# Performance work log

Hardware: AMD Instinct MI355X
Metric: run time of the kernel (lower is better)

The kernel has to match this reference:

```python
import jax, jax.numpy as jnp
import numpy as np

N_NODES = 50000
N_EDGES = 400000
D_IN = 512
D_OUT = 512
MASK_RATE = 0.3


def setup_inputs() -> dict:
    key = jax.random.key(0)
    k1, k2, k3, k4, k5 = jax.random.split(key, 5)
    feat = jax.random.normal(k1, (N_NODES, D_IN), dtype=jnp.float32)
    # xavier_uniform for weight [in_feat, out_feat]
    limit = float(np.sqrt(6.0 / (D_IN + D_OUT)))
    weight = jax.random.uniform(k2, (D_IN, D_OUT), dtype=jnp.float32, minval=-limit, maxval=limit)
    edge_src = jax.random.randint(k3, (N_EDGES,), 0, N_NODES, dtype=jnp.int64 if jax.config.jax_enable_x64 else jnp.int32)
    edge_dst = jax.random.randint(k4, (N_EDGES,), 0, N_NODES, dtype=jnp.int64 if jax.config.jax_enable_x64 else jnp.int32)
    edge_val = jax.random.uniform(k5, (N_EDGES,), dtype=jnp.float32)
    # deterministic stand-in for torch.randperm(...)[:num_mask]
    perm = jax.random.permutation(jax.random.fold_in(key, 7), N_NODES)
    mask_idx = perm[: int(MASK_RATE * N_NODES)]
    return {
        "feat": feat,
        "weight": weight,
        "edge_val": edge_val,
        "edge_src": edge_src,
        "edge_dst": edge_dst,
        "mask_idx": mask_idx,
    }


def reference(feat, weight, edge_val, edge_src, edge_dst, mask_idx):
    # zero out masked node rows (encoding_mask_noise)
    out_x = feat.at[mask_idx].set(0.0)
    # dense transform: [N, D_in] @ [D_in, D_out]
    x = out_x @ weight
    # spmm(adj, x): for edge (src -> dst, val): out[dst] += val * x[src]
    msgs = edge_val[:, None] * x[edge_src]  # [E, D_out]
    out = jax.ops.segment_sum(msgs, edge_dst, num_segments=feat.shape[0])
    return out, mask_idx
```

## Files before the change

### kernel.cpp

```cpp
#include <hip/hip_runtime.h>

#define DD 512
#define SCAN_B 256
#define BM 128
#define BN 128
#define BK 32
#define NSTEP 16
typedef unsigned short u16;
typedef unsigned int u32;
typedef unsigned char u8;

typedef __attribute__((ext_vector_type(8))) __bf16 bf16v8;
typedef __attribute__((ext_vector_type(2))) __bf16 bf16v2;
typedef __attribute__((ext_vector_type(4))) float f32x4;

__device__ __forceinline__ u32 pk2(float a, float b) {
  bf16v2 v;
  v[0] = (__bf16)a;
  v[1] = (__bf16)b;
  return __builtin_bit_cast(u32, v);
}
__device__ __forceinline__ u16 f2bf(float f) {
  return __builtin_bit_cast(u16, (__bf16)f);
}
__device__ __forceinline__ float bf2f(u32 h) {
  return __builtin_bit_cast(float, h << 16);
}

typedef const __attribute__((address_space(1))) void* gptr_t;
typedef __attribute__((address_space(3))) void* lptr_t;
__device__ __forceinline__ void gload_lds16(const void* g, void* l) {
  __builtin_amdgcn_global_load_lds((gptr_t)g, (lptr_t)l, 16, 0, 0);
}

#define BAR_N(N)                                                        \
  do {                                                                  \
    __builtin_amdgcn_sched_barrier(0);                                  \
    asm volatile("s_waitcnt vmcnt(" #N ") lgkmcnt(0)\n\ts_barrier" ::: "memory"); \
  } while (0)

__global__ __launch_bounds__(256) void wconv_t(const float* __restrict__ W,
                                               u16* __restrict__ Wt) {
  __shared__ float sm[64][65];
  const int bx = blockIdx.x;
  const int by = blockIdx.y;
  const int t = threadIdx.x;
  const int r = t >> 6;
  const int c = t & 63;
#pragma unroll
  for (int i = 0; i < 64; i += 4)
    sm[i + r][c] = W[(size_t)(bx * 64 + i + r) * DD + by * 64 + c];
  __syncthreads();
#pragma unroll
  for (int i = 0; i < 64; i += 4) {
    const int n = by * 64 + i + r;
    const int k = bx * 64 + c;
    Wt[(size_t)n * DD + k] = f2bf(sm[c][i + r]);
  }
}

__global__ __launch_bounds__(512) void gemm_pipe(const float* __restrict__ A,
                                                 const u16* __restrict__ Bt,
                                                 u16* __restrict__ X,
                                                 const u8* __restrict__ flg, int M) {
  __shared__ __align__(16) u16 ldsA[2][BM * BK];
  __shared__ __align__(16) u16 ldsB[3][BN * BK];
  const int tid = threadIdx.x;
  const int lane = tid & 63;
  const int w = tid >> 6;
  const int wm = w >> 2;
  const int wn = w & 3;

  const int nwg = gridDim.x;
  const int b = blockIdx.x;
  const int xcd = b & 7, j = b >> 3;
  const int q = nwg >> 3, r_ = nwg & 7;
  const int unit = (xcd < r_ ? xcd * (q + 1) : r_ * (q + 1) + (xcd - r_) * q) + j;
  const int row0 = (unit >> 2) * BM;
  const int colB = (unit & 3) * BN;

  const int lr = lane & 15;
  const int kg = lane >> 4;

  f32x4 acc[4][2] = {};

  const int arow = tid >> 2;
  const int agk = (tid & 3) ^ ((arow >> 1) & 3);
  int ar = row0 + arow;
  if (ar >= M) ar = M - 1;
  const float* gA = A + (size_t)ar * DD + agk * 8;
  const int laoff = tid * 8;
  const u32 akeep = flg[ar] ? 0u : 0xFFFFFFFFu;

  const int bcol = tid >> 2;
  const int bgk = (tid & 3) ^ ((bcol >> 1) & 3);
  const u16* gB = Bt + (size_t)(colB + bcol) * DD + bgk * 8;
  const int lboff = tid * 8;

  f32x4 rP[2][2];

  gload_lds16(gB, &ldsB[0][lboff]);
  gload_lds16(gB + BK, &ldsB[1][lboff]);
  rP[0][0] = *(const f32x4*)(gA);
  rP[0][1] = *(const f32x4*)(gA + 4);
  rP[1][0] = *(const f32x4*)(gA + BK);
  rP[1][1] = *(const f32x4*)(gA + BK + 4);
  {
    uint4 pk;
    pk.x = pk2(rP[0][0].x, rP[0][0].y) & akeep;
    pk.y = pk2(rP[0][0].z, rP[0][0].w) & akeep;
    pk.z = pk2(rP[0][1].x, rP[0][1].y) & akeep;
    pk.w = pk2(rP[0][1].z, rP[0][1].w) & akeep;
    *(uint4*)&ldsA[0][laoff] = pk;
  }
  BAR_N(2);

#pragma unroll
  for (int t = 0; t < NSTEP; ++t) {
    if (t + 2 < NSTEP)
      gload_lds16(gB + (t + 2) * BK, &ldsB[(t + 2) % 3][lboff]);
    if (t + 2 < NSTEP) {
      rP[t & 1][0] = *(const f32x4*)(gA + (t + 2) * BK);
      rP[t & 1][1] = *(const f32x4*)(gA + (t + 2) * BK + 4);
    }
    __builtin_amdgcn_sched_barrier(0);

    bf16v8 af[4], bfr[2];
#pragma unroll
    for (int m = 0; m < 4; ++m) {
      const int row = wm * 64 + m * 16 + lr;
      const int kc = kg ^ ((row >> 1) & 3);
      af[m] = *(const bf16v8*)&ldsA[t & 1][row * BK + kc * 8];
    }
#pragma unroll
    for (int n = 0; n < 2; ++n) {
      const int col = wn * 32 + n * 16 + lr;
      const int kc = kg ^ ((col >> 1) & 3);
      bfr[n] = *(const bf16v8*)&ldsB[t % 3][col * BK + kc * 8];
    }
#pragma unroll
    for (int m = 0; m < 4; ++m)
#pragma unroll
      for (int n = 0; n < 2; ++n)
        acc[m][n] = __builtin_amdgcn_mfma_f32_16x16x32_bf16(af[m], bfr[n], acc[m][n], 0, 0, 0);

    if (t + 1 < NSTEP) {
      uint4 pk;
      pk.x = pk2(rP[(t + 1) & 1][0].x, rP[(t + 1) & 1][0].y) & akeep;
      pk.y = pk2(rP[(t + 1) & 1][0].z, rP[(t + 1) & 1][0].w) & akeep;
      pk.z = pk2(rP[(t + 1) & 1][1].x, rP[(t + 1) & 1][1].y) & akeep;
      pk.w = pk2(rP[(t + 1) & 1][1].z, rP[(t + 1) & 1][1].w) & akeep;
      *(uint4*)&ldsA[(t + 1) & 1][laoff] = pk;
    }

    if (t < NSTEP - 3)      BAR_N(3);
    else if (t < NSTEP - 1) BAR_N(0);
  }

  const int crow = (lane >> 4) * 4;
  const int ccol = lane & 15;
#pragma unroll
  for (int m = 0; m < 4; ++m) {
    const int rowb = row0 + wm * 64 + m * 16 + crow;
#pragma unroll
    for (int n = 0; n < 2; ++n) {
      const int col = colB + wn * 32 + n * 16 + ccol;
#pragma unroll
      for (int r = 0; r < 4; ++r)
        X[(size_t)(rowb + r) * DD + col] = f2bf(acc[m][n][r]);
    }
  }
}

__global__ __launch_bounds__(256) void flag_build(const int* __restrict__ mask,
                                                  u8* __restrict__ flg,
                                                  float* __restrict__ out_tail, int nm) {
  const int i = blockIdx.x * blockDim.x + threadIdx.x;
  if (i < nm) {
    const int r = mask[i];
    flg[r] = 1;
    out_tail[i] = (float)r;
  }
}

__global__ __launch_bounds__(256) void hist(const int* __restrict__ dst,
                                            int* __restrict__ counts, int n) {
  const int i = blockIdx.x * blockDim.x + threadIdx.x;
  if (i < n) atomicAdd(&counts[dst[i]], 1);
}

__global__ __launch_bounds__(SCAN_B) void scanA(const int* __restrict__ counts,
                                                int* __restrict__ lscan,
                                                int* __restrict__ blockSums, int n) {
  __shared__ int sm[SCAN_B];
  const int t = threadIdx.x;
  const int i = blockIdx.x * SCAN_B + t;
  const int v = (i < n) ? counts[i] : 0;
  sm[t] = v;
  __syncthreads();
  for (int off = 1; off < SCAN_B; off <<= 1) {
    int add = (t >= off) ? sm[t - off] : 0;
    __syncthreads();
    sm[t] += add;
    __syncthreads();
  }
  if (i < n) lscan[i] = sm[t] - v;
  if (t == SCAN_B - 1) blockSums[blockIdx.x] = sm[t];
}

__global__ __launch_bounds__(SCAN_B) void scanC(int* __restrict__ lscan,
                                                const int* __restrict__ blockSums,
                                                int* __restrict__ cursor, int n, int nb) {
  __shared__ int sm[SCAN_B];
  const int t = threadIdx.x;
  const int v = (t < nb) ? blockSums[t] : 0;
  sm[t] = v;
  __syncthreads();
  for (int off = 1; off < SCAN_B; off <<= 1) {
    int add = (t >= off) ? sm[t - off] : 0;
    __syncthreads();
    sm[t] += add;
    __syncthreads();
  }
  const int base = sm[blockIdx.x] - ((blockIdx.x < nb) ? blockSums[blockIdx.x] : 0);
  const int i = blockIdx.x * SCAN_B + t;
  if (i < n) {
    const int o = lscan[i] + base;
    lscan[i] = o;
    cursor[i] = o;
  }
}

__global__ __launch_bounds__(256) void scatter_sort(const int* __restrict__ src,
                                                    const int* __restrict__ dst,
                                                    const float* __restrict__ ev,
                                                    int* __restrict__ cursor,
                                                    int* __restrict__ ssrc,
                                                    float* __restrict__ sval, int n) {
  const int i = blockIdx.x * blockDim.x + threadIdx.x;
  if (i < n) {
    const int pos = atomicAdd(&cursor[dst[i]], 1);
    ssrc[pos] = src[i];
    sval[pos] = ev[i];
  }
}

__global__ __launch_bounds__(256) void aggregate(const u16* __restrict__ x,
                                                 const int* __restrict__ ssrc,
                                                 const float* __restrict__ sval,
                                                 const int* __restrict__ offsets,
                                                 const int* __restrict__ counts,
                                                 float* __restrict__ out, int n_nodes) {
  const int node = blockIdx.x * 4 + (threadIdx.x >> 6);
  if (node >= n_nodes) return;
  const int lane = threadIdx.x & 63;
  const int b = offsets[node];
  const int e = b + counts[node];
  float acc[8] = {};
  int j = b;
#define AGG1(U, V)                                      \
  do {                                                  \
    acc[0] = fmaf(V, bf2f(U.x & 0xffffu), acc[0]);      \
    acc[1] = fmaf(V, bf2f(U.x >> 16),     acc[1]);      \
    acc[2] = fmaf(V, bf2f(U.y & 0xffffu), acc[2]);      \
    acc[3] = fmaf(V, bf2f(U.y >> 16),     acc[3]);      \
    acc[4] = fmaf(V, bf2f(U.z & 0xffffu), acc[4]);      \
    acc[5] = fmaf(V, bf2f(U.z >> 16),     acc[5]);      \
    acc[6] = fmaf(V, bf2f(U.w & 0xffffu), acc[6]);      \
    acc[7] = fmaf(V, bf2f(U.w >> 16),     acc[7]);      \
  } while (0)
  for (; j + 4 <= e; j += 4) {
    const int s0 = ssrc[j], s1 = ssrc[j + 1], s2 = ssrc[j + 2], s3 = ssrc[j + 3];
    const float v0 = sval[j], v1 = sval[j + 1], v2 = sval[j + 2], v3 = sval[j + 3];
    const uint4 u0 = *(const uint4*)(x + (size_t)s0 * DD + lane * 8);
    const uint4 u1 = *(const uint4*)(x + (size_t)s1 * DD + lane * 8);
    const uint4 u2 = *(const uint4*)(x + (size_t)s2 * DD + lane * 8);
    const uint4 u3 = *(const uint4*)(x + (size_t)s3 * DD + lane * 8);
    AGG1(u0, v0); AGG1(u1, v1); AGG1(u2, v2); AGG1(u3, v3);
  }
  for (; j < e; ++j) {
    const int s = ssrc[j];
    const float v = sval[j];
    const uint4 u = *(const uint4*)(x + (size_t)s * DD + lane * 8);
    AGG1(u, v);
  }
#undef AGG1
  f32x4* o = (f32x4*)(out + (size_t)node * DD + lane * 8);
  f32x4 o0 = {acc[0], acc[1], acc[2], acc[3]};
  f32x4 o1 = {acc[4], acc[5], acc[6], acc[7]};
  __builtin_nontemporal_store(o0, o);
  __builtin_nontemporal_store(o1, o + 1);
}

extern "C" void kernel_launch(void* const* d_in, const int* in_sizes, int n_in,
                              void* d_out, int out_size, void* d_ws, size_t ws_size,
                              hipStream_t stream) {
  const float* feat     = (const float*)d_in[0];
  const float* weight   = (const float*)d_in[1];
  const float* edge_val = (const float*)d_in[2];
  const int*   edge_src = (const int*)d_in[3];
  const int*   edge_dst = (const int*)d_in[4];
  const int*   mask_idx = (const int*)d_in[5];

  const int n_nodes = in_sizes[0] / DD;
  const int n_edges = in_sizes[2];
  const int n_mask  = in_sizes[5];

  const int n_tiles_m = (n_nodes + BM - 1) / BM;
  const int m_pad = n_tiles_m * BM;

  float* out = (float*)d_out;

  char* base = (char*)d_ws;
  size_t off = 0;
  auto alloc = [&](size_t bytes) {
    void* p = base + off;
    off = (off + bytes + 255) & ~(size_t)255;
    return p;
  };
  u16*   x      = (u16*)alloc((size_t)m_pad * DD * sizeof(u16));
  u16*   wt     = (u16*)alloc((size_t)DD * DD * sizeof(u16));
  int*   counts = (int*)alloc((size_t)n_nodes * sizeof(int));
  u8*    flg    = (u8*)alloc((size_t)m_pad);
  const size_t zspan = (size_t)((char*)(flg + m_pad) - (char*)counts);
  int*   offs   = (int*)alloc((size_t)n_nodes * sizeof(int));
  int*   cursor = (int*)alloc((size_t)n_nodes * sizeof(int));
  int*   bsums  = (int*)alloc(SCAN_B * sizeof(int));
  int*   ssrc   = (int*)alloc((size_t)n_edges * sizeof(int));
  float* sval   = (float*)alloc((size_t)n_edges * sizeof(float));

  const int nb = (n_nodes + SCAN_B - 1) / SCAN_B;

  (void)hipMemsetAsync(counts, 0, zspan, stream);
  hist<<<(n_edges + 255) / 256, 256, 0, stream>>>(edge_dst, counts, n_edges);
  scanA<<<nb, SCAN_B, 0, stream>>>(counts, offs, bsums, n_nodes);
  scanC<<<nb, SCAN_B, 0, stream>>>(offs, bsums, cursor, n_nodes, nb);
  scatter_sort<<<(n_edges + 255) / 256, 256, 0, stream>>>(edge_src, edge_dst, edge_val,
                                                          cursor, ssrc, sval, n_edges);
  flag_build<<<(n_mask + 255) / 256, 256, 0, stream>>>(mask_idx, flg,
                                                       out + (size_t)n_nodes * DD, n_mask);

  dim3 wg(DD / 64, DD / 64);
  wconv_t<<<wg, 256, 0, stream>>>(weight, wt);
  const int nwg = (DD / BN) * n_tiles_m;
  gemm_pipe<<<nwg, 512, 0, stream>>>(feat, wt, x, flg, n_nodes);

  aggregate<<<(n_nodes + 3) / 4, 256, 0, stream>>>(x, ssrc, sval, offs, counts, out, n_nodes);
}
```

Baseline: 179.9 us.

## Load GEMM B fragments directly from global, pack edges, fuse hist and flag kernels

The GEMM no longer stages the transposed weight tile in LDS. Each wave reads its B fragments straight from global memory into registers, and the A prefetch ring grows to three slots with a shallower barrier wait. Launch bounds now ask for higher occupancy. Edge src and val are packed into one int2 array so the aggregate does a single load per edge and unrolls by 8 for more gathers in flight. The histogram and mask-flag kernels are fused into one launch. The risk is uncoalesced, redundant global B reads (each wave rereads B with no LDS sharing) and more register pressure.

```diff
diff --git a/kernel.cpp b/kernel.cpp
--- a/kernel.cpp
+++ b/kernel.cpp
@@ -27,12 +27,6 @@
   return __builtin_bit_cast(float, h << 16);
 }
 
-typedef const __attribute__((address_space(1))) void* gptr_t;
-typedef __attribute__((address_space(3))) void* lptr_t;
-__device__ __forceinline__ void gload_lds16(const void* g, void* l) {
-  __builtin_amdgcn_global_load_lds((gptr_t)g, (lptr_t)l, 16, 0, 0);
-}
-
 #define BAR_N(N)                                                        \
   do {                                                                  \
     __builtin_amdgcn_sched_barrier(0);                                  \
@@ -59,12 +53,11 @@
   }
 }
 
-__global__ __launch_bounds__(512) void gemm_pipe(const float* __restrict__ A,
-                                                 const u16* __restrict__ Bt,
-                                                 u16* __restrict__ X,
-                                                 const u8* __restrict__ flg, int M) {
+__global__ __launch_bounds__(512, 4) void gemm_pipe(const float* __restrict__ A,
+                                                    const u16* __restrict__ Bt,
+                                                    u16* __restrict__ X,
+                                                    const u8* __restrict__ flg, int M) {
   __shared__ __align__(16) u16 ldsA[2][BM * BK];
-  __shared__ __align__(16) u16 ldsB[3][BN * BK];
   const int tid = threadIdx.x;
   const int lane = tid & 63;
   const int w = tid >> 6;
@@ -73,9 +66,9 @@
 
   const int nwg = gridDim.x;
   const int b = blockIdx.x;
-  const int xcd = b & 7, j = b >> 3;
+  const int xcd = b & 7, jj = b >> 3;
   const int q = nwg >> 3, r_ = nwg & 7;
-  const int unit = (xcd < r_ ? xcd * (q + 1) : r_ * (q + 1) + (xcd - r_) * q) + j;
+  const int unit = (xcd < r_ ? xcd * (q + 1) : r_ * (q + 1) + (xcd - r_) * q) + jj;
   const int row0 = (unit >> 2) * BM;
   const int colB = (unit & 3) * BN;
 
@@ -92,15 +85,11 @@
   const int laoff = tid * 8;
   const u32 akeep = flg[ar] ? 0u : 0xFFFFFFFFu;
 
-  const int bcol = tid >> 2;
-  const int bgk = (tid & 3) ^ ((bcol >> 1) & 3);
-  const u16* gB = Bt + (size_t)(colB + bcol) * DD + bgk * 8;
-  const int lboff = tid * 8;
-
-  f32x4 rP[2][2];
-
-  gload_lds16(gB, &ldsB[0][lboff]);
-  gload_lds16(gB + BK, &ldsB[1][lboff]);
+  const u16* gB0 = Bt + (size_t)(colB + wn * 32 + lr) * DD + kg * 8;
+  const u16* gB1 = Bt + (size_t)(colB + wn * 32 + 16 + lr) * DD + kg * 8;
+
+  f32x4 rP[3][2];
+
   rP[0][0] = *(const f32x4*)(gA);
   rP[0][1] = *(const f32x4*)(gA + 4);
   rP[1][0] = *(const f32x4*)(gA + BK);
@@ -117,15 +106,16 @@
 
 #pragma unroll
   for (int t = 0; t < NSTEP; ++t) {
-    if (t + 2 < NSTEP)
-      gload_lds16(gB + (t + 2) * BK, &ldsB[(t + 2) % 3][lboff]);
+    bf16v8 bfr[2];
+    bfr[0] = *(const bf16v8*)(gB0 + t * BK);
+    bfr[1] = *(const bf16v8*)(gB1 + t * BK);
+
     if (t + 2 < NSTEP) {
-      rP[t & 1][0] = *(const f32x4*)(gA + (t + 2) * BK);
-      rP[t & 1][1] = *(const f32x4*)(gA + (t + 2) * BK + 4);
+      rP[(t + 2) % 3][0] = *(const f32x4*)(gA + (t + 2) * BK);
+      rP[(t + 2) % 3][1] = *(const f32x4*)(gA + (t + 2) * BK + 4);
     }
-    __builtin_amdgcn_sched_barrier(0);
-
-    bf16v8 af[4], bfr[2];
+
+    bf16v8 af[4];
 #pragma unroll
     for (int m = 0; m < 4; ++m) {
       const int row = wm * 64 + m * 16 + lr;
@@ -133,27 +123,23 @@
       af[m] = *(const bf16v8*)&ldsA[t & 1][row * BK + kc * 8];
     }
 #pragma unroll
-    for (int n = 0; n < 2; ++n) {
-      const int col = wn * 32 + n * 16 + lr;
-      const int kc = kg ^ ((col >> 1) & 3);
-      bfr[n] = *(const bf16v8*)&ldsB[t % 3][col * BK + kc * 8];
-    }
-#pragma unroll
     for (int m = 0; m < 4; ++m)
 #pragma unroll
       for (int n = 0; n < 2; ++n)
         acc[m][n] = __builtin_amdgcn_mfma_f32_16x16x32_bf16(af[m], bfr[n], acc[m][n], 0, 0, 0);
 
     if (t + 1 < NSTEP) {
+      const f32x4 p0 = rP[(t + 1) % 3][0];
+      const f32x4 p1 = rP[(t + 1) % 3][1];
       uint4 pk;
-      pk.x = pk2(rP[(t + 1) & 1][0].x, rP[(t + 1) & 1][0].y) & akeep;
-      pk.y = pk2(rP[(t + 1) & 1][0].z, rP[(t + 1) & 1][0].w) & akeep;
-      pk.z = pk2(rP[(t + 1) & 1][1].x, rP[(t + 1) & 1][1].y) & akeep;
-      pk.w = pk2(rP[(t + 1) & 1][1].z, rP[(t + 1) & 1][1].w) & akeep;
+      pk.x = pk2(p0.x, p0.y) & akeep;
+      pk.y = pk2(p0.z, p0.w) & akeep;
+      pk.z = pk2(p1.x, p1.y) & akeep;
+      pk.w = pk2(p1.z, p1.w) & akeep;
       *(uint4*)&ldsA[(t + 1) & 1][laoff] = pk;
     }
 
-    if (t < NSTEP - 3)      BAR_N(3);
+    if (t < NSTEP - 2)      BAR_N(2);
     else if (t < NSTEP - 1) BAR_N(0);
   }
 
@@ -172,21 +158,19 @@
   }
 }
 
-__global__ __launch_bounds__(256) void flag_build(const int* __restrict__ mask,
-                                                  u8* __restrict__ flg,
-                                                  float* __restrict__ out_tail, int nm) {
+__global__ __launch_bounds__(256) void hist_flag(const int* __restrict__ dst,
+                                                 int* __restrict__ counts,
+                                                 const int* __restrict__ mask,
+                                                 u8* __restrict__ flg,
+                                                 float* __restrict__ out_tail,
+                                                 int n, int nm) {
   const int i = blockIdx.x * blockDim.x + threadIdx.x;
+  if (i < n) atomicAdd(&counts[dst[i]], 1);
   if (i < nm) {
     const int r = mask[i];
     flg[r] = 1;
     out_tail[i] = (float)r;
   }
-}
-
-__global__ __launch_bounds__(256) void hist(const int* __restrict__ dst,
-                                            int* __restrict__ counts, int n) {
-  const int i = blockIdx.x * blockDim.x + threadIdx.x;
-  if (i < n) atomicAdd(&counts[dst[i]], 1);
 }
 
 __global__ __launch_bounds__(SCAN_B) void scanA(const int* __restrict__ counts,
@@ -235,19 +219,16 @@
                                                     const int* __restrict__ dst,
                                                     const float* __restrict__ ev,
                                                     int* __restrict__ cursor,
-                                                    int* __restrict__ ssrc,
-                                                    float* __restrict__ sval, int n) {
+                                                    int2* __restrict__ esp, int n) {
   const int i = blockIdx.x * blockDim.x + threadIdx.x;
   if (i < n) {
     const int pos = atomicAdd(&cursor[dst[i]], 1);
-    ssrc[pos] = src[i];
-    sval[pos] = ev[i];
+    esp[pos] = make_int2(src[i], __float_as_int(ev[i]));
   }
 }
 
 __global__ __launch_bounds__(256) void aggregate(const u16* __restrict__ x,
-                                                 const int* __restrict__ ssrc,
-                                                 const float* __restrict__ sval,
+                                                 const int2* __restrict__ esp,
                                                  const int* __restrict__ offsets,
                                                  const int* __restrict__ counts,
                                                  float* __restrict__ out, int n_nodes) {
@@ -269,20 +250,32 @@
     acc[6] = fmaf(V, bf2f(U.w & 0xffffu), acc[6]);      \
     acc[7] = fmaf(V, bf2f(U.w >> 16),     acc[7]);      \
   } while (0)
+  for (; j + 8 <= e; j += 8) {
+    int2 p[8];
+    uint4 u[8];
+#pragma unroll
+    for (int k = 0; k < 8; ++k) p[k] = esp[j + k];
+#pragma unroll
+    for (int k = 0; k < 8; ++k)
+      u[k] = *(const uint4*)(x + (size_t)p[k].x * DD + lane * 8);
+#pragma unroll
+    for (int k = 0; k < 8; ++k) AGG1(u[k], __int_as_float(p[k].y));
+  }
   for (; j + 4 <= e; j += 4) {
-    const int s0 = ssrc[j], s1 = ssrc[j + 1], s2 = ssrc[j + 2], s3 = ssrc[j + 3];
-    const float v0 = sval[j], v1 = sval[j + 1], v2 = sval[j + 2], v3 = sval[j + 3];
-    const uint4 u0 = *(const uint4*)(x + (size_t)s0 * DD + lane * 8);
-    const uint4 u1 = *(const uint4*)(x + (size_t)s1 * DD + lane * 8);
-    const uint4 u2 = *(const uint4*)(x + (size_t)s2 * DD + lane * 8);
-    const uint4 u3 = *(const uint4*)(x + (size_t)s3 * DD + lane * 8);
-    AGG1(u0, v0); AGG1(u1, v1); AGG1(u2, v2); AGG1(u3, v3);
+    const int2 p0 = esp[j], p1 = esp[j + 1], p2 = esp[j + 2], p3 = esp[j + 3];
+    const uint4 u0 = *(const uint4*)(x + (size_t)p0.x * DD + lane * 8);
+    const uint4 u1 = *(const uint4*)(x + (size_t)p1.x * DD + lane * 8);
+    const uint4 u2 = *(const uint4*)(x + (size_t)p2.x * DD + lane * 8);
+    const uint4 u3 = *(const uint4*)(x + (size_t)p3.x * DD + lane * 8);
+    AGG1(u0, __int_as_float(p0.y));
+    AGG1(u1, __int_as_float(p1.y));
+    AGG1(u2, __int_as_float(p2.y));
+    AGG1(u3, __int_as_float(p3.y));
   }
   for (; j < e; ++j) {
-    const int s = ssrc[j];
-    const float v = sval[j];
-    const uint4 u = *(const uint4*)(x + (size_t)s * DD + lane * 8);
-    AGG1(u, v);
+    const int2 p = esp[j];
+    const uint4 u = *(const uint4*)(x + (size_t)p.x * DD + lane * 8);
+    AGG1(u, __int_as_float(p.y));
   }
 #undef AGG1
   f32x4* o = (f32x4*)(out + (size_t)node * DD + lane * 8);
@@ -326,24 +319,23 @@
   int*   offs   = (int*)alloc((size_t)n_nodes * sizeof(int));
   int*   cursor = (int*)alloc((size_t)n_nodes * sizeof(int));
   int*   bsums  = (int*)alloc(SCAN_B * sizeof(int));
-  int*   ssrc   = (int*)alloc((size_t)n_edges * sizeof(int));
-  float* sval   = (float*)alloc((size_t)n_edges * sizeof(float));
+  int2*  esp    = (int2*)alloc((size_t)n_edges * sizeof(int2));
 
   const int nb = (n_nodes + SCAN_B - 1) / SCAN_B;
 
   (void)hipMemsetAsync(counts, 0, zspan, stream);
-  hist<<<(n_edges + 255) / 256, 256, 0, stream>>>(edge_dst, counts, n_edges);
+  hist_flag<<<(n_edges + 255) / 256, 256, 0, stream>>>(edge_dst, counts, mask_idx, flg,
+                                                       out + (size_t)n_nodes * DD,
+                                                       n_edges, n_mask);
   scanA<<<nb, SCAN_B, 0, stream>>>(counts, offs, bsums, n_nodes);
   scanC<<<nb, SCAN_B, 0, stream>>>(offs, bsums, cursor, n_nodes, nb);
   scatter_sort<<<(n_edges + 255) / 256, 256, 0, stream>>>(edge_src, edge_dst, edge_val,
-                                                          cursor, ssrc, sval, n_edges);
-  flag_build<<<(n_mask + 255) / 256, 256, 0, stream>>>(mask_idx, flg,
-                                                       out + (size_t)n_nodes * DD, n_mask);
+                                                          cursor, esp, n_edges);
 
   dim3 wg(DD / 64, DD / 64);
   wconv_t<<<wg, 256, 0, stream>>>(weight, wt);
   const int nwg = (DD / BN) * n_tiles_m;
   gemm_pipe<<<nwg, 512, 0, stream>>>(feat, wt, x, flg, n_nodes);
 
-  aggregate<<<(n_nodes + 3) / 4, 256, 0, stream>>>(x, ssrc, sval, offs, counts, out, n_nodes);
-}
+  aggregate<<<(n_nodes + 3) / 4, 256, 0, stream>>>(x, esp, offs, counts, out, n_nodes);
+}
```

After: 202.0 us. 12.3% more time.
